# Performance work log

Hardware: AMD Instinct MI355X
Metric: run time of the kernel (lower is better)

Reference implementation:

```python
import jax, jax.numpy as jnp
import numpy as np
import math

H = 1024
HEADS = 32
S = 4096
B = 3
E = 8192
QA = 2049  # start of QA span; content sentences cover [1, 2049)


def setup_inputs() -> dict:
    key = jax.random.key(0)
    ks = jax.random.split(key, 12)
    hidden_states = jax.random.normal(ks[0], (B, S, H), dtype=jnp.float32)
    st_mask = jax.random.randint(ks[1], (B, S), 0, 2, dtype=jnp.int64)
    edges_src = jax.random.randint(ks[2], (E,), 0, S, dtype=jnp.int64)
    edges_tgt = jax.random.randint(ks[3], (E,), 0, S, dtype=jnp.int64)
    edges_type = jax.random.randint(ks[4], (E,), 0, 26, dtype=jnp.int64)
    edges_pos = jax.random.randint(ks[5], (E,), 0, S, dtype=jnp.int64)
    # 32 content sentences of length 64 covering [1, 2049), then the QA span (2049, 4096)
    begins = 1 + 64 * np.arange(32)
    ends = begins + 64
    pairs = np.stack([np.append(begins, QA), np.append(ends, S)], axis=1).reshape(-1)
    all_sen = np.tile(pairs, (B, 1)).astype(np.int64)  # kept as numpy: static span indices
    scale = 0.02
    Wq = jax.random.normal(ks[6], (H, H), jnp.float32) * scale
    Wk = jax.random.normal(ks[7], (H, H), jnp.float32) * scale
    Wv = jax.random.normal(ks[8], (H, H), jnp.float32) * scale
    Wo = jax.random.normal(ks[9], (H, H), jnp.float32) * scale
    bq = jnp.zeros((H,), jnp.float32)
    bk = jnp.zeros((H,), jnp.float32)
    bv = jnp.zeros((H,), jnp.float32)
    bo = jnp.zeros((H,), jnp.float32)
    return dict(hidden_states=hidden_states, st_mask=st_mask, edges_src=edges_src,
                edges_tgt=edges_tgt, edges_type=edges_type, edges_pos=edges_pos,
                all_sen=all_sen, Wq=Wq, bq=bq, Wk=Wk, bk=bk, Wv=Wv, bv=bv, Wo=Wo, bo=bo)


def reference(hidden_states, st_mask, edges_src, edges_tgt, edges_type, edges_pos,
              all_sen, Wq, bq, Wk, bk, Wv, bv, Wo, bo):
    h = HEADS
    d_model = hidden_states.shape[-1]
    dk = d_model // h
    inv_sqrt_dk = 1.0 / math.sqrt(dk)

    def mha(q, k, v):
        # q: [Lq, H]; k, v: [Lk, H] -> [Lq, H]  (dropout is identity in eval mode)
        q2 = (q @ Wq.T + bq).reshape(-1, h, dk).transpose(1, 0, 2)  # [h, Lq, dk]
        k2 = (k @ Wk.T + bk).reshape(-1, h, dk).transpose(1, 0, 2)  # [h, Lk, dk]
        v2 = (v @ Wv.T + bv).reshape(-1, h, dk).transpose(1, 0, 2)
        scores = jnp.einsum('hqd,hkd->hqk', q2, k2) * inv_sqrt_dk
        p = jax.nn.softmax(scores, axis=-1)
        x = jnp.einsum('hqk,hkd->hqd', p, v2).transpose(1, 0, 2).reshape(-1, d_model)
        return x @ Wo.T + bo

    sen = np.asarray(all_sen)  # static span indices (host constants)
    outs = []
    for i in range(hidden_states.shape[0]):  # fixed small batch of 3
        pairs = sen[i][sen[i] != -1].reshape(-1, 2)
        qa, end = int(pairs[-1, 0]), int(pairs[-1, 1])
        q = hidden_states[i, 1:qa]       # [qa-1, H]
        kv = hidden_states[i, qa:end]    # [end-qa, H]
        hq1q2 = mha(q, kv, kv)           # content attends to QA span
        hq2q1 = mha(kv, q, q)            # QA span attends to content
        # hidden_states2 analogue: zeros elsewhere, attended reps in the two spans
        row = jnp.zeros_like(hidden_states[i])
        row = row.at[1:qa].set(hq1q2).at[qa:end].set(hq2q1)
        # per-sentence means (hidden_states3)
        sent_means = jnp.stack([row[b:e].mean(axis=0) for b, e in pairs])  # [n_sen, H]
        V11 = sent_means[:-1].mean(axis=0)  # mean over content-sentence means
        V21 = sent_means[-1]                # QA-span mean
        outs.append(jnp.concatenate([V11, V21]))
    return jnp.stack(outs)  # [3, 2H]
```

## Files before the change

### kernel.cpp

```cpp
#include <hip/hip_runtime.h>
#include <cstddef>

typedef __attribute__((ext_vector_type(8))) short bf16x8;
typedef __attribute__((ext_vector_type(4))) float f32x4;
typedef __attribute__((ext_vector_type(4))) unsigned short u16x4;
typedef __attribute__((ext_vector_type(8))) unsigned short u16x8;

namespace {
constexpr int B_ = 3, S_ = 4096, H_ = 1024, NH_ = 32;
constexpr int SEG1 = 1, SEG2 = 2049;
constexpr int NQ1 = 2048, NK1 = 2047, NQ2 = 2047, NK2 = 2048;
constexpr float SCALE = 0.17677669529663687f;
constexpr float LOG2E = 1.4426950408889634f;
constexpr float QSC   = SCALE * LOG2E;

constexpr size_t oXb = 0;
constexpr size_t oWb = oXb + (size_t)12288 * 1024 * 2;
constexpr size_t oBB = oWb + (size_t)2048 * 1024 * 2;
constexpr size_t oQH = oBB + (size_t)2048 * 4;
constexpr size_t oKH = oQH + (size_t)6 * 32 * 2048 * 32 * 2;
constexpr size_t oNL = oKH + (size_t)6 * 32 * 2048 * 32 * 2;
constexpr size_t oCS = oNL + (size_t)6 * 2048 * 4;
constexpr size_t oU  = oCS + (size_t)6 * 32 * 2048 * 4;
constexpr size_t oMv = oU  + (size_t)6 * 32 * 1024 * 4;
constexpr size_t oUP = oMv + (size_t)6 * 1024 * 4;
}

#if __has_builtin(__builtin_amdgcn_exp2f)
#define EXP2(x) __builtin_amdgcn_exp2f(x)
#else
#define EXP2(x) exp2f(x)
#endif
#if __has_builtin(__builtin_amdgcn_logf)
#define LOG2(x) __builtin_amdgcn_logf(x)
#else
#define LOG2(x) log2f(x)
#endif

__device__ __forceinline__ unsigned short f2bf(float f) {
    unsigned u = __float_as_uint(f);
    u += 0x7FFF + ((u >> 16) & 1);
    return (unsigned short)(u >> 16);
}
__device__ __forceinline__ float bf2f(unsigned short u) {
    return __uint_as_float((unsigned)u << 16);
}
__device__ __forceinline__ void gl16(const unsigned short* gp, unsigned short* lp) {
    __builtin_amdgcn_global_load_lds(
        (const __attribute__((address_space(1))) unsigned int*)gp,
        (__attribute__((address_space(3))) unsigned int*)lp, 16, 0, 0);
}

__global__ __launch_bounds__(256) void conv_x(const float* __restrict__ X,
                                              unsigned short* __restrict__ Xb)
{
    const size_t i4 = (size_t)blockIdx.x * 256 + threadIdx.x;
    const float4 v = *(const float4*)&X[i4 * 4];
    u16x4 o;
    o[0] = f2bf(v.x); o[1] = f2bf(v.y); o[2] = f2bf(v.z); o[3] = f2bf(v.w);
    *(u16x4*)&Xb[i4 * 4] = o;
}

__global__ __launch_bounds__(256) void conv_w(const float* __restrict__ Wq,
                                              const float* __restrict__ bq,
                                              const float* __restrict__ Wk,
                                              const float* __restrict__ bk,
                                              unsigned short* __restrict__ Wb,
                                              float* __restrict__ bb,
                                              unsigned short* __restrict__ QH,
                                              unsigned short* __restrict__ KH)
{
    const int i4 = blockIdx.x * 256 + threadIdx.x;
    const int base = i4 * 4;
    const bool isQ = base < (1 << 20);
    const float sc = isQ ? QSC : 1.f;
    const float* src = isQ ? &Wq[base] : &Wk[base - (1 << 20)];
    const float4 v = *(const float4*)src;
    u16x4 o;
    o[0] = f2bf(v.x * sc); o[1] = f2bf(v.y * sc);
    o[2] = f2bf(v.z * sc); o[3] = f2bf(v.w * sc);
    *(u16x4*)&Wb[base] = o;
    if (base < 2048) {
#pragma unroll
        for (int c = 0; c < 4; ++c) {
            const int j = base + c;
            bb[j] = (j < 1024) ? QSC * bq[j] : bk[j - 1024];
        }
    }
    if (i4 < 3072) {
        const int b = i4 >> 10, rem = i4 & 1023, h = rem >> 5, c = rem & 31;
        QH[(((size_t)(b * 2 + 1) * NH_ + h) * 2048 + 2047) * 32 + c] = 0;
        KH[(((size_t)(b * 2 + 0) * NH_ + h) * 2048 + 2047) * 32 + c] = 0;
    }
}

__global__ __launch_bounds__(256) void proj_mfma(const unsigned short* __restrict__ Xb,
                                                 const unsigned short* __restrict__ Wb,
                                                 const float* __restrict__ bb,
                                                 unsigned short* __restrict__ QH,
                                                 unsigned short* __restrict__ KH)
{
    __shared__ unsigned short ldsX[2][4096];
    __shared__ unsigned short ldsW[2][4096];
    const int tid = threadIdx.x;
    const int lane = tid & 63, w = tid >> 6;
    const int m0 = blockIdx.x * 128;
    const int n0 = blockIdx.y * 128;
    const int cr = (w >> 1) * 64;
    const int xc = (w & 1) * 64;

    const int co = ((lane & 3) ^ ((lane >> 3) & 3)) * 8;
    const unsigned short* gX = Xb + (size_t)(m0 + 32 * w + (lane >> 2)) * 1024 + co;
    const unsigned short* gW = Wb + (size_t)(n0 + 32 * w + (lane >> 2)) * 1024 + co;

#define STAGE(K0, BUF) do { \
    gl16(gX + (K0),             &ldsX[BUF][(32 * w) * 32]); \
    gl16(gX + (K0) + 16 * 1024, &ldsX[BUF][(32 * w + 16) * 32]); \
    gl16(gW + (K0),             &ldsW[BUF][(32 * w) * 32]); \
    gl16(gW + (K0) + 16 * 1024, &ldsW[BUF][(32 * w + 16) * 32]); \
} while (0)

    const int lr = lane & 15, lg = lane >> 4;
    const int mrW = cr + lr, mrX = xc + lr;
    const int oW = mrW * 32 + ((lg ^ ((mrW >> 1) & 3)) * 8);
    const int oX = mrX * 32 + ((lg ^ ((mrX >> 1) & 3)) * 8);

    f32x4 acc[4][4] = {};
    STAGE(0, 0);
    asm volatile("s_waitcnt vmcnt(0)" ::: "memory");
    __syncthreads();

    for (int kt = 0; kt < 32; ++kt) {
        const int buf = kt & 1;
        if (kt < 31) STAGE((kt + 1) * 32, buf ^ 1);
        bf16x8 wf[4], xf[4];
#pragma unroll
        for (int i = 0; i < 4; ++i) wf[i] = *(const bf16x8*)&ldsW[buf][oW + i * 512];
#pragma unroll
        for (int j = 0; j < 4; ++j) xf[j] = *(const bf16x8*)&ldsX[buf][oX + j * 512];
#pragma unroll
        for (int i = 0; i < 4; ++i)
#pragma unroll
            for (int j = 0; j < 4; ++j)
                acc[i][j] = __builtin_amdgcn_mfma_f32_16x16x32_bf16(wf[i], xf[j], acc[i][j], 0, 0, 0);
        asm volatile("s_waitcnt vmcnt(0)" ::: "memory");
        __syncthreads();
    }
#undef STAGE

    const bool sideK = (n0 >= 1024);
    unsigned short* dst = sideK ? KH : QH;

    int rowoff[4];
#pragma unroll
    for (int j = 0; j < 4; ++j) {
        const int g = m0 + xc + 16 * j + lr;
        const int b = g >> 12, rr = g & 4095;
        int v = -1;
        if (rr >= 2049) {
            const int seg = b * 2 + (sideK ? 0 : 1);
            v = seg * (NH_ * 2048 * 32) + (rr - 2049) * 32;
        } else if (rr >= 1) {
            const int seg = b * 2 + (sideK ? 1 : 0);
            v = seg * (NH_ * 2048 * 32) + (rr - 1) * 32;
        }
        rowoff[j] = v;
    }

    int coloff[4]; f32x4 bias4[4];
#pragma unroll
    for (int i = 0; i < 4; ++i) {
        const int c = n0 + cr + 16 * i + lg * 4;
        const int local = c - (sideK ? 1024 : 0);
        coloff[i] = (local >> 5) * (2048 * 32) + (local & 31);
        bias4[i] = *(const f32x4*)&bb[c];
    }

#pragma unroll
    for (int j = 0; j < 4; ++j) {
        if (rowoff[j] < 0) continue;
#pragma unroll
        for (int i = 0; i < 4; ++i) {
            u16x4 o;
#pragma unroll
            for (int r = 0; r < 4; ++r) o[r] = f2bf(acc[i][j][r] + bias4[i][r]);
            *(u16x4*)&dst[(size_t)rowoff[j] + coloff[i]] = o;
        }
    }
}

__global__ __launch_bounds__(256) void zpass(const unsigned short* __restrict__ QH,
                                             const unsigned short* __restrict__ KH,
                                             float* __restrict__ NL)
{
    const int tid = threadIdx.x, lane = tid & 63, w = tid >> 6;
    const int bm = blockIdx.z, mha = bm & 1;
    const int h = blockIdx.y;
    const int nq = mha ? NQ2 : NQ1, nk = mha ? NK2 : NK1;
    const size_t panel = ((size_t)bm * NH_ + h) * 2048 * 32;
    const int lr = lane & 15, lg = lane >> 4;
    const int q0 = blockIdx.x * 256 + w * 64;
    const f32x4 zero = {0.f, 0.f, 0.f, 0.f};

    const unsigned short* Qp = QH + panel + (size_t)(q0 + lr) * 32 + lg * 8;
    const unsigned short* Kp = KH + panel + (size_t)lr * 32 + lg * 8;

    bf16x8 a[4];
#pragma unroll
    for (int i = 0; i < 4; ++i) a[i] = *(const bf16x8*)(Qp + i * 16 * 32);

    f32x4 z[4] = {zero, zero, zero, zero};
    for (int kt = 0; kt < 127; ++kt) {
        const bf16x8 kb = *(const bf16x8*)(Kp + (size_t)kt * 16 * 32);
#pragma unroll
        for (int i = 0; i < 4; ++i) {
            const f32x4 d = __builtin_amdgcn_mfma_f32_16x16x32_bf16(a[i], kb, zero, 0, 0, 0);
            f32x4 e;
#pragma unroll
            for (int r = 0; r < 4; ++r) e[r] = EXP2(d[r]);
            z[i] += e;
        }
    }
    {
        const bf16x8 kb = *(const bf16x8*)(Kp + (size_t)127 * 16 * 32);
        const float m = (2032 + lr < nk) ? 1.f : 0.f;
#pragma unroll
        for (int i = 0; i < 4; ++i) {
            const f32x4 d = __builtin_amdgcn_mfma_f32_16x16x32_bf16(a[i], kb, zero, 0, 0, 0);
            f32x4 e;
#pragma unroll
            for (int r = 0; r < 4; ++r) e[r] = m * EXP2(d[r]);
            z[i] += e;
        }
    }

#pragma unroll
    for (int i = 0; i < 4; ++i) {
        f32x4 zi = z[i];
#pragma unroll
        for (int r = 0; r < 4; ++r) {
            float v = zi[r];
            v += __shfl_xor(v, 1, 64);
            v += __shfl_xor(v, 2, 64);
            v += __shfl_xor(v, 4, 64);
            v += __shfl_xor(v, 8, 64);
            zi[r] = v;
        }
        if (lr == 0) {
            const int qb = q0 + i * 16 + lg * 4;
            f32x4 o;
#pragma unroll
            for (int r = 0; r < 4; ++r)
                o[r] = (qb + r < nq) ? -LOG2(zi[r]) : -1e30f;
            *(f32x4*)&NL[(size_t)bm * 2048 + qb] = o;
        }
    }
}

__global__ __launch_bounds__(256) void colsum(const unsigned short* __restrict__ QH,
                                              const unsigned short* __restrict__ KH,
                                              const float* __restrict__ NL,
                                              float* __restrict__ CS)
{
    const int tid = threadIdx.x, lane = tid & 63, w = tid >> 6;
    const int bm = blockIdx.z, mha = bm & 1;
    const int h = blockIdx.y;
    const int nk = mha ? NK2 : NK1;
    const size_t panel = ((size_t)bm * NH_ + h) * 2048 * 32;
    const int lr = lane & 15, lg = lane >> 4;
    const int kc = blockIdx.x * 256 + w * 64;
    const f32x4 zero = {0.f, 0.f, 0.f, 0.f};

    const unsigned short* Kp = KH + panel + (size_t)(kc + lr) * 32 + lg * 8;
    const unsigned short* Qp = QH + panel + (size_t)lr * 32 + lg * 8;
    const float* zp = NL + (size_t)bm * 2048 + lg * 4;

    bf16x8 kb[4];
#pragma unroll
    for (int j = 0; j < 4; ++j) kb[j] = *(const bf16x8*)(Kp + j * 16 * 32);

    f32x4 cacc[4] = {zero, zero, zero, zero};
    for (int qt = 0; qt < 128; ++qt) {
        const bf16x8 ai = *(const bf16x8*)(Qp + (size_t)qt * 16 * 32);
        const f32x4 cv = *(const f32x4*)(zp + qt * 16);
#pragma unroll
        for (int j = 0; j < 4; ++j) {
            const f32x4 d = __builtin_amdgcn_mfma_f32_16x16x32_bf16(ai, kb[j], cv, 0, 0, 0);
            f32x4 e;
#pragma unroll
            for (int r = 0; r < 4; ++r) e[r] = EXP2(d[r]);
            cacc[j] += e;
        }
    }

#pragma unroll
    for (int j = 0; j < 4; ++j) {
        float v = (cacc[j][0] + cacc[j][1]) + (cacc[j][2] + cacc[j][3]);
        v += __shfl_xor(v, 16, 64);
        v += __shfl_xor(v, 32, 64);
        const int col = kc + 16 * j + lr;
        if (lane < 16 && col < nk)
            CS[((size_t)bm * NH_ + h) * 2048 + col] = v;
    }
}

__global__ __launch_bounds__(256) void colsum_x(
    const unsigned short* __restrict__ Xb, const float* __restrict__ CS,
    float* __restrict__ UP)
{
    __shared__ float sl[8][128];
    const int tid = threadIdx.x;
    const int bm = blockIdx.z;
    const int b = bm >> 1, mha = bm & 1;
    const int kbase = mha ? SEG1 : SEG2;
    const int nk = mha ? NK2 : NK1;
    const int kt = blockIdx.x;
    const int k0 = kt * 128;
    const int hg = blockIdx.y * 8;

    for (int idx = tid; idx < 8 * 128; idx += 256) {
        const int hh = idx >> 7, kk = idx & 127;
        const int k = k0 + kk;
        sl[hh][kk] = (k < nk) ? CS[((size_t)bm * NH_ + hg + hh) * 2048 + k] : 0.f;
    }
    __syncthreads();

    float acc[8][4] = {};
    const int c4 = tid * 4;
#pragma unroll 4
    for (int kk = 0; kk < 128; ++kk) {
        const int k = k0 + kk;
        const int krow = (k < nk) ? k : 0;
        const u16x4 xv = *(const u16x4*)&Xb[((size_t)b * S_ + kbase + krow) * H_ + c4];
        const float x0 = bf2f(xv[0]), x1 = bf2f(xv[1]), x2 = bf2f(xv[2]), x3 = bf2f(xv[3]);
#pragma unroll
        for (int hh = 0; hh < 8; ++hh) {
            const float sv = sl[hh][kk];
            acc[hh][0] += sv * x0; acc[hh][1] += sv * x1;
            acc[hh][2] += sv * x2; acc[hh][3] += sv * x3;
        }
    }
#pragma unroll
    for (int hh = 0; hh < 8; ++hh) {
        f32x4 o; o[0] = acc[hh][0]; o[1] = acc[hh][1]; o[2] = acc[hh][2]; o[3] = acc[hh][3];
        *(f32x4*)&UP[((size_t)(bm * NH_ + hg + hh) * 16 + kt) * 1024 + c4] = o;
    }
}

__global__ __launch_bounds__(256) void reduce_u(const float* __restrict__ UP,
                                                float* __restrict__ U)
{
    const int gid = blockIdx.x * 256 + threadIdx.x;
    const int row = gid >> 8;
    const int c4 = (gid & 255) * 4;
    const float* p = UP + (size_t)row * 16 * 1024 + c4;
    f32x4 s = *(const f32x4*)p;
#pragma unroll
    for (int t = 1; t < 16; ++t) s += *(const f32x4*)(p + t * 1024);
    *(f32x4*)&U[(size_t)row * 1024 + c4] = s;
}

__global__ __launch_bounds__(256) void compute_m(
    const float* __restrict__ U, const float* __restrict__ Wv,
    const float* __restrict__ bv, float* __restrict__ Mvec)
{
    const int bm = blockIdx.y;
    const int mha = bm & 1;
    const float invnq = 1.f / (float)(mha ? NQ2 : NQ1);
    const int o = blockIdx.x * 256 + threadIdx.x;
    const int hh = o >> 5;
    const float* u = &U[((size_t)bm * NH_ + hh) * H_];
    const float* w = &Wv[(size_t)o * H_];
    float acc = 0.f;
    for (int in = 0; in < H_; in += 4) {
        const float4 uv = *(const float4*)&u[in];
        const float4 wv = *(const float4*)&w[in];
        acc += uv.x * wv.x + uv.y * wv.y + uv.z * wv.z + uv.w * wv.w;
    }
    Mvec[(size_t)bm * H_ + o] = acc * invnq + bv[o];
}

__global__ __launch_bounds__(256) void final_out(
    const float* __restrict__ Mvec, const float* __restrict__ Wo,
    const float* __restrict__ bo, float* __restrict__ out)
{
    const int bm = blockIdx.y;
    const int b = bm >> 1, mha = bm & 1;
    const int o = blockIdx.x * 256 + threadIdx.x;
    const float* mv = &Mvec[(size_t)bm * H_];
    const float* w = &Wo[(size_t)o * H_];
    float acc = 0.f;
    for (int in = 0; in < H_; in += 4) {
        const float4 mvv = *(const float4*)&mv[in];
        const float4 wv = *(const float4*)&w[in];
        acc += mvv.x * wv.x + mvv.y * wv.y + mvv.z * wv.z + mvv.w * wv.w;
    }
    out[(size_t)b * 2048 + mha * 1024 + o] = acc + bo[o];
}

extern "C" void kernel_launch(void* const* d_in, const int* in_sizes, int n_in,
                              void* d_out, int out_size, void* d_ws, size_t ws_size,
                              hipStream_t stream)
{
    const float* hidden = (const float*)d_in[0];
    const float* Wq = (const float*)d_in[7];
    const float* bq = (const float*)d_in[8];
    const float* Wk = (const float*)d_in[9];
    const float* bk = (const float*)d_in[10];
    const float* Wv = (const float*)d_in[11];
    const float* bv = (const float*)d_in[12];
    const float* Wo = (const float*)d_in[13];
    const float* bo = (const float*)d_in[14];
    float* out = (float*)d_out;
    char* ws = (char*)d_ws;

    unsigned short* Xb  = (unsigned short*)(ws + oXb);
    unsigned short* Wb  = (unsigned short*)(ws + oWb);
    float* bb           = (float*)(ws + oBB);
    unsigned short* QHp = (unsigned short*)(ws + oQH);
    unsigned short* KHp = (unsigned short*)(ws + oKH);
    float* NL           = (float*)(ws + oNL);
    float* CS           = (float*)(ws + oCS);
    float* U            = (float*)(ws + oU);
    float* Mv           = (float*)(ws + oMv);
    float* UP           = (float*)(ws + oUP);

    const dim3 blk(256);
    conv_x<<<12288, blk, 0, stream>>>(hidden, Xb);
    conv_w<<<2048, blk, 0, stream>>>(Wq, bq, Wk, bk, Wb, bb, QHp, KHp);
    proj_mfma<<<dim3(96, 16), blk, 0, stream>>>(Xb, Wb, bb, QHp, KHp);
    zpass<<<dim3(8, 32, 6), blk, 0, stream>>>(QHp, KHp, NL);
    colsum<<<dim3(8, 32, 6), blk, 0, stream>>>(QHp, KHp, NL, CS);
    colsum_x<<<dim3(16, 4, 6), blk, 0, stream>>>(Xb, CS, UP);
    reduce_u<<<192, blk, 0, stream>>>(UP, U);
    compute_m<<<dim3(4, 6), blk, 0, stream>>>(U, Wv, bv, Mv);
    final_out<<<dim3(4, 6), blk, 0, stream>>>(Mv, Wo, bo, out);
}
```

Before: 418.6 us.

## Triple-buffer projection GEMM and software-prefetch K/Q tiles in score kernels

The projection GEMM moves from double to triple LDS buffering. It issues global loads two k-steps ahead, waits with partial vmcnt, and uses a raw s_barrier with sched_barrier in place of a full drain and __syncthreads each iteration. The row-normalizer and column-sum kernels unroll their inner loops by two and register-prefetch the next K/Q fragments and normalizer vectors, so global load latency overlaps MFMA and exp work. This raises LDS use to 48KB per block and increases register pressure, which may lower occupancy.

```diff
diff --git a/kernel.cpp b/kernel.cpp
--- a/kernel.cpp
+++ b/kernel.cpp
@@ -100,8 +100,8 @@
                                                  unsigned short* __restrict__ QH,
                                                  unsigned short* __restrict__ KH)
 {
-    __shared__ unsigned short ldsX[2][4096];
-    __shared__ unsigned short ldsW[2][4096];
+    __shared__ unsigned short ldsX[3 * 4096];
+    __shared__ unsigned short ldsW[3 * 4096];
     const int tid = threadIdx.x;
     const int lane = tid & 63, w = tid >> 6;
     const int m0 = blockIdx.x * 128;
@@ -114,10 +114,10 @@
     const unsigned short* gW = Wb + (size_t)(n0 + 32 * w + (lane >> 2)) * 1024 + co;
 
 #define STAGE(K0, BUF) do { \
-    gl16(gX + (K0),             &ldsX[BUF][(32 * w) * 32]); \
-    gl16(gX + (K0) + 16 * 1024, &ldsX[BUF][(32 * w + 16) * 32]); \
-    gl16(gW + (K0),             &ldsW[BUF][(32 * w) * 32]); \
-    gl16(gW + (K0) + 16 * 1024, &ldsW[BUF][(32 * w + 16) * 32]); \
+    gl16(gX + (K0),             &ldsX[(BUF) * 4096 + (32 * w) * 32]); \
+    gl16(gX + (K0) + 16 * 1024, &ldsX[(BUF) * 4096 + (32 * w + 16) * 32]); \
+    gl16(gW + (K0),             &ldsW[(BUF) * 4096 + (32 * w) * 32]); \
+    gl16(gW + (K0) + 16 * 1024, &ldsW[(BUF) * 4096 + (32 * w + 16) * 32]); \
 } while (0)
 
     const int lr = lane & 15, lg = lane >> 4;
@@ -127,24 +127,31 @@
 
     f32x4 acc[4][4] = {};
     STAGE(0, 0);
-    asm volatile("s_waitcnt vmcnt(0)" ::: "memory");
-    __syncthreads();
-
+    STAGE(32, 1);
+    asm volatile("s_waitcnt vmcnt(4)" ::: "memory");
+    __builtin_amdgcn_s_barrier();
+    __builtin_amdgcn_sched_barrier(0);
+
+    int cur = 0, stg = 2;
     for (int kt = 0; kt < 32; ++kt) {
-        const int buf = kt & 1;
-        if (kt < 31) STAGE((kt + 1) * 32, buf ^ 1);
+        const int cb = cur * 4096;
         bf16x8 wf[4], xf[4];
 #pragma unroll
-        for (int i = 0; i < 4; ++i) wf[i] = *(const bf16x8*)&ldsW[buf][oW + i * 512];
-#pragma unroll
-        for (int j = 0; j < 4; ++j) xf[j] = *(const bf16x8*)&ldsX[buf][oX + j * 512];
+        for (int i = 0; i < 4; ++i) wf[i] = *(const bf16x8*)&ldsW[cb + oW + i * 512];
+#pragma unroll
+        for (int j = 0; j < 4; ++j) xf[j] = *(const bf16x8*)&ldsX[cb + oX + j * 512];
+        if (kt + 2 < 32) STAGE((kt + 2) * 32, stg);
 #pragma unroll
         for (int i = 0; i < 4; ++i)
 #pragma unroll
             for (int j = 0; j < 4; ++j)
                 acc[i][j] = __builtin_amdgcn_mfma_f32_16x16x32_bf16(wf[i], xf[j], acc[i][j], 0, 0, 0);
-        asm volatile("s_waitcnt vmcnt(0)" ::: "memory");
-        __syncthreads();
+        if (kt + 2 < 32) asm volatile("s_waitcnt vmcnt(4) lgkmcnt(0)" ::: "memory");
+        else             asm volatile("s_waitcnt vmcnt(0) lgkmcnt(0)" ::: "memory");
+        __builtin_amdgcn_s_barrier();
+        __builtin_amdgcn_sched_barrier(0);
+        cur = (cur == 2) ? 0 : cur + 1;
+        stg = (stg == 2) ? 0 : stg + 1;
     }
 #undef STAGE
 
@@ -209,24 +216,44 @@
 #pragma unroll
     for (int i = 0; i < 4; ++i) a[i] = *(const bf16x8*)(Qp + i * 16 * 32);
 
+    bf16x8 kb0 = *(const bf16x8*)(Kp);
+    bf16x8 kb1 = *(const bf16x8*)(Kp + 512);
+
     f32x4 z[4] = {zero, zero, zero, zero};
-    for (int kt = 0; kt < 127; ++kt) {
-        const bf16x8 kb = *(const bf16x8*)(Kp + (size_t)kt * 16 * 32);
+    for (int kt = 0; kt < 126; kt += 2) {
+        const bf16x8 n0 = *(const bf16x8*)(Kp + (size_t)(kt + 2) * 512);
+        const bf16x8 n1 = *(const bf16x8*)(Kp + (size_t)(kt + 3) * 512);
 #pragma unroll
         for (int i = 0; i < 4; ++i) {
-            const f32x4 d = __builtin_amdgcn_mfma_f32_16x16x32_bf16(a[i], kb, zero, 0, 0, 0);
+            const f32x4 d = __builtin_amdgcn_mfma_f32_16x16x32_bf16(a[i], kb0, zero, 0, 0, 0);
             f32x4 e;
 #pragma unroll
             for (int r = 0; r < 4; ++r) e[r] = EXP2(d[r]);
             z[i] += e;
         }
+#pragma unroll
+        for (int i = 0; i < 4; ++i) {
+            const f32x4 d = __builtin_amdgcn_mfma_f32_16x16x32_bf16(a[i], kb1, zero, 0, 0, 0);
+            f32x4 e;
+#pragma unroll
+            for (int r = 0; r < 4; ++r) e[r] = EXP2(d[r]);
+            z[i] += e;
+        }
+        kb0 = n0; kb1 = n1;
+    }
+#pragma unroll
+    for (int i = 0; i < 4; ++i) {
+        const f32x4 d = __builtin_amdgcn_mfma_f32_16x16x32_bf16(a[i], kb0, zero, 0, 0, 0);
+        f32x4 e;
+#pragma unroll
+        for (int r = 0; r < 4; ++r) e[r] = EXP2(d[r]);
+        z[i] += e;
     }
     {
-        const bf16x8 kb = *(const bf16x8*)(Kp + (size_t)127 * 16 * 32);
         const float m = (2032 + lr < nk) ? 1.f : 0.f;
 #pragma unroll
         for (int i = 0; i < 4; ++i) {
-            const f32x4 d = __builtin_amdgcn_mfma_f32_16x16x32_bf16(a[i], kb, zero, 0, 0, 0);
+            const f32x4 d = __builtin_amdgcn_mfma_f32_16x16x32_bf16(a[i], kb1, zero, 0, 0, 0);
             f32x4 e;
 #pragma unroll
             for (int r = 0; r < 4; ++r) e[r] = m * EXP2(d[r]);
@@ -279,18 +306,50 @@
 #pragma unroll
     for (int j = 0; j < 4; ++j) kb[j] = *(const bf16x8*)(Kp + j * 16 * 32);
 
+    bf16x8 ai0 = *(const bf16x8*)(Qp);
+    f32x4  cv0 = *(const f32x4*)(zp);
+    bf16x8 ai1 = *(const bf16x8*)(Qp + 512);
+    f32x4  cv1 = *(const f32x4*)(zp + 16);
+
     f32x4 cacc[4] = {zero, zero, zero, zero};
-    for (int qt = 0; qt < 128; ++qt) {
-        const bf16x8 ai = *(const bf16x8*)(Qp + (size_t)qt * 16 * 32);
-        const f32x4 cv = *(const f32x4*)(zp + qt * 16);
+    for (int qt = 0; qt < 126; qt += 2) {
+        const bf16x8 an0 = *(const bf16x8*)(Qp + (size_t)(qt + 2) * 512);
+        const f32x4  cn0 = *(const f32x4*)(zp + (qt + 2) * 16);
+        const bf16x8 an1 = *(const bf16x8*)(Qp + (size_t)(qt + 3) * 512);
+        const f32x4  cn1 = *(const f32x4*)(zp + (qt + 3) * 16);
 #pragma unroll
         for (int j = 0; j < 4; ++j) {
-            const f32x4 d = __builtin_amdgcn_mfma_f32_16x16x32_bf16(ai, kb[j], cv, 0, 0, 0);
+            const f32x4 d = __builtin_amdgcn_mfma_f32_16x16x32_bf16(ai0, kb[j], cv0, 0, 0, 0);
             f32x4 e;
 #pragma unroll
             for (int r = 0; r < 4; ++r) e[r] = EXP2(d[r]);
             cacc[j] += e;
         }
+#pragma unroll
+        for (int j = 0; j < 4; ++j) {
+            const f32x4 d = __builtin_amdgcn_mfma_f32_16x16x32_bf16(ai1, kb[j], cv1, 0, 0, 0);
+            f32x4 e;
+#pragma unroll
+            for (int r = 0; r < 4; ++r) e[r] = EXP2(d[r]);
+            cacc[j] += e;
+        }
+        ai0 = an0; cv0 = cn0; ai1 = an1; cv1 = cn1;
+    }
+#pragma unroll
+    for (int j = 0; j < 4; ++j) {
+        const f32x4 d = __builtin_amdgcn_mfma_f32_16x16x32_bf16(ai0, kb[j], cv0, 0, 0, 0);
+        f32x4 e;
+#pragma unroll
+        for (int r = 0; r < 4; ++r) e[r] = EXP2(d[r]);
+        cacc[j] += e;
+    }
+#pragma unroll
+    for (int j = 0; j < 4; ++j) {
+        const f32x4 d = __builtin_amdgcn_mfma_f32_16x16x32_bf16(ai1, kb[j], cv1, 0, 0, 0);
+        f32x4 e;
+#pragma unroll
+        for (int r = 0; r < 4; ++r) e[r] = EXP2(d[r]);
+        cacc[j] += e;
     }
 
 #pragma unroll
```

Result: faster. 378.7 us (-9.5%).
